# Kernel optimization log

Measured on AMD Instinct MI355X. Metric: run time of the kernel, lower is better.

Reference implementation:

```python
import jax, jax.numpy as jnp
import numpy as np

DIM = 768
HEADS = 12
HID = 3072  # mlp_ratio * dim
BATCH = 8
FRAMES = 16
GRID = 14
NTOK = GRID * GRID
LN_EPS = 1e-5
EPS = 1e-6


def setup_inputs() -> dict:
    key = jax.random.key(0)
    ks = jax.random.split(key, 8)
    w = lambda k, shape: jax.random.normal(k, shape, jnp.float32) * 0.02
    return {
        "x": jax.random.normal(ks[0], (BATCH * FRAMES, NTOK, DIM), jnp.float32),
        "ln1_w": jnp.ones((DIM,), jnp.float32),
        "ln1_b": jnp.zeros((DIM,), jnp.float32),
        "qkv_w": w(ks[1], (3 * DIM, DIM)),
        "proj_w": w(ks[2], (DIM, DIM)),
        "proj_b": jnp.zeros((DIM,), jnp.float32),
        "ln2_w": jnp.ones((DIM,), jnp.float32),
        "ln2_b": jnp.zeros((DIM,), jnp.float32),
        "fc1_w": w(ks[3], (HID, DIM)),
        "fc1_b": jnp.zeros((HID,), jnp.float32),
        "dw_w": w(ks[4], (HID, 1, 3, 3)),
        "dw_b": jnp.zeros((HID,), jnp.float32),
        "fc2_w": w(ks[5], (DIM, HID)),
        "fc2_b": jnp.zeros((DIM,), jnp.float32),
        "H": GRID,
        "W": GRID,
        "num_frames": FRAMES,
    }


def _layernorm(x, w, b):
    mu = jnp.mean(x, axis=-1, keepdims=True)
    var = jnp.mean(jnp.square(x - mu), axis=-1, keepdims=True)
    return (x - mu) * jax.lax.rsqrt(var + LN_EPS) * w + b


def _joint_ts_attention(xn, qkv_w, proj_w, proj_b, num_frames):
    # xn: (b*f, n, c)
    Bt, n, C = xn.shape
    h = HEADS
    e = C // h
    scale = e ** (-0.5)
    qkv = jnp.einsum('bnc,dc->bnd', xn, qkv_w).reshape(Bt, n, 3, h, e)
    q, k, v = qkv[:, :, 0], qkv[:, :, 1], qkv[:, :, 2]
    # ReLU feature map + scale offset
    q_ = jax.nn.relu(q) + scale
    k_ = jax.nn.relu(k) + scale
    b = Bt // num_frames
    m = num_frames * n  # joint time-space sequence length
    q_ = q_.reshape(b, m, h, e)
    k_ = k_.reshape(b, m, h, e)
    v_ = v.reshape(b, m, h, e)
    # kv_: (b, h, e, e)
    kv = jnp.einsum('bnhe,bnhd->bhed', k_, v_)
    k_sum = jnp.sum(k_, axis=1)  # (b, h, e)
    z = 1.0 / (jnp.einsum('bnhe,bhe->bnh', q_, k_sum) + EPS)  # (b, m, h)
    out = jnp.einsum('bnhe,bhed->bnhd', q_, kv) * z[..., None]  # (b, m, h, e)
    out = out.reshape(Bt, n, C)
    return jnp.einsum('bnc,dc->bnd', out, proj_w) + proj_b


def _dwconv(x, w, b, H, W):
    # x: (B, N, C) -> NCHW depthwise 3x3, pad 1
    Bn, n, c = x.shape
    xi = jnp.transpose(x, (0, 2, 1)).reshape(Bn, c, H, W)
    y = jax.lax.conv_general_dilated(
        xi, w, window_strides=(1, 1), padding=((1, 1), (1, 1)),
        dimension_numbers=('NCHW', 'OIHW', 'NCHW'), feature_group_count=c)
    y = y + b[None, :, None, None]
    return jnp.transpose(y.reshape(Bn, c, n), (0, 2, 1))


def reference(x, ln1_w, ln1_b, qkv_w, proj_w, proj_b, ln2_w, ln2_b,
              fc1_w, fc1_b, dw_w, dw_b, fc2_w, fc2_b, H, W, num_frames):
    # x = x + attn(norm1(x), num_frames)
    x = x + _joint_ts_attention(_layernorm(x, ln1_w, ln1_b), qkv_w, proj_w, proj_b, num_frames)
    # x = x + mlp(norm2(x), H, W)
    xn = _layernorm(x, ln2_w, ln2_b)
    hdn = jnp.einsum('bnc,hc->bnh', xn, fc1_w) + fc1_b
    hdn = _dwconv(hdn, dw_w, dw_b, H, W)
    hdn = jax.nn.gelu(hdn, approximate=False)
    out = jnp.einsum('bnh,ch->bnc', hdn, fc2_w) + fc2_b
    return x + out
```

## Files before the change

kernel.cpp:

```cpp
#include <hip/hip_runtime.h>

typedef unsigned short u16;
typedef unsigned int u32;

typedef __bf16 bf16x8 __attribute__((ext_vector_type(8)));
typedef float f32x4 __attribute__((ext_vector_type(4)));

#define DIM 768
#define HID 3072
#define NTOK 196
#define BT 128
#define NTOKENS (BT * NTOK)
#define MJ 3136
#define HEADS 12

#define SZ_WB   ((size_t)(2304*768 + 768*768 + 3072*768 + 768*3072) * 2)
#define SZ_XN   ((size_t)NTOKENS * DIM * 2)
#define SZ_QKV  ((size_t)NTOKENS * 2304 * 2)
#define SZ_X2   ((size_t)NTOKENS * DIM * 4)
#define SZ_HDN  ((size_t)NTOKENS * HID * 2)
#define SZ_KV   ((size_t)96 * 4096 * 4)
#define SZ_KS   ((size_t)96 * 64 * 4)
#define WS_NEED (SZ_WB + SZ_XN + SZ_QKV + SZ_X2 + SZ_HDN + SZ_KV + SZ_KS)

static void* g_buf = nullptr;

__device__ __forceinline__ float b2f(u16 u) {
  union { u32 i; float f; } x; x.i = ((u32)u) << 16; return x.f;
}
__device__ __forceinline__ u16 f2b(float f) {
  u32 x = __float_as_uint(f);
  return (u16)((x + 0x7fffu + ((x >> 16) & 1u)) >> 16);
}

__device__ __forceinline__ void gload_lds16(const u16* g, u16* l) {
  __builtin_amdgcn_global_load_lds(
      (const __attribute__((address_space(1))) u32*)g,
      (__attribute__((address_space(3))) u32*)l, 16, 0, 0);
}

__global__ __launch_bounds__(256) void cvt_f32_bf16(const float* __restrict__ in,
    u16* __restrict__ out, int n4)
{
  int i = blockIdx.x * 256 + threadIdx.x;
  if (i < n4) {
    float4 f = ((const float4*)in)[i];
    ushort4 r;
    r.x = f2b(f.x); r.y = f2b(f.y); r.z = f2b(f.z); r.w = f2b(f.w);
    ((ushort4*)out)[i] = r;
  }
}

__global__ __launch_bounds__(256) void zero_f32(float* __restrict__ p, int n) {
  int i = blockIdx.x * 256 + threadIdx.x;
  if (i < n) p[i] = 0.0f;
}

__global__ __launch_bounds__(256) void ln_kernel(const float* __restrict__ xin,
    const float* __restrict__ w, const float* __restrict__ b, u16* __restrict__ out)
{
  const int token = blockIdx.x * 4 + (threadIdx.x >> 6);
  const int lane = threadIdx.x & 63;
  float v[12];
  const float* x = xin + (size_t)token * DIM;
#pragma unroll
  for (int c = 0; c < 3; ++c) {
    float4 f = *(const float4*)(x + c * 256 + lane * 4);
    v[c*4+0] = f.x; v[c*4+1] = f.y; v[c*4+2] = f.z; v[c*4+3] = f.w;
  }
  float s = 0.f, sq = 0.f;
#pragma unroll
  for (int i = 0; i < 12; ++i) { s += v[i]; sq += v[i] * v[i]; }
#pragma unroll
  for (int off = 32; off > 0; off >>= 1) {
    s += __shfl_xor(s, off, 64);
    sq += __shfl_xor(sq, off, 64);
  }
  const float mean = s * (1.0f / 768.0f);
  const float var = sq * (1.0f / 768.0f) - mean * mean;
  const float rstd = rsqrtf(var + 1e-5f);
  u16* o = out + (size_t)token * DIM;
#pragma unroll
  for (int c = 0; c < 3; ++c) {
    float4 wv = *(const float4*)(w + c * 256 + lane * 4);
    float4 bv = *(const float4*)(b + c * 256 + lane * 4);
    ushort4 r;
    r.x = f2b((v[c*4+0] - mean) * rstd * wv.x + bv.x);
    r.y = f2b((v[c*4+1] - mean) * rstd * wv.y + bv.y);
    r.z = f2b((v[c*4+2] - mean) * rstd * wv.z + bv.z);
    r.w = f2b((v[c*4+3] - mean) * rstd * wv.w + bv.w);
    *(ushort4*)(o + c * 256 + lane * 4) = r;
  }
}

template<int MODE, int NXT, int NN, int KK>
__global__ __launch_bounds__(512, 2) void gemm8(
    const u16* __restrict__ A, const u16* __restrict__ W,
    const float* __restrict__ bias, const float* __restrict__ res,
    void* __restrict__ out)
{
  extern __shared__ char smem[];
  u16* As = (u16*)smem;
  u16* Bs = (u16*)(smem + 65536);

  const int t = threadIdx.x;
  const int l = t & 63;
  const int w = t >> 6;
  const int wm = w >> 2;
  const int wn = w & 3;

  constexpr int TOTAL = 98 * NXT;
  constexpr int Q8 = TOTAL >> 3;
  constexpr int R8 = TOTAL & 7;
  const int orig = blockIdx.x;
  const int xcd = orig & 7;
  const int idx = orig >> 3;
  const int wg = (xcd < R8) ? (xcd * (Q8 + 1) + idx)
                            : (R8 * (Q8 + 1) + (xcd - R8) * Q8 + idx);
  const int m0 = (wg / NXT) * 256;
  const int n0 = (wg % NXT) * 256;

  const int srow = w * 16 + (l >> 3);
  const int scol = ((l & 7) ^ (l >> 3)) * 8;
  const u16* gA = A + (size_t)(m0 + srow) * KK + scol;
  const u16* gB = W + (size_t)(n0 + srow) * KK + scol;
  u16* lA = As + w * 1024;
  u16* lB = Bs + w * 1024;

#define STAGE_A(bb, h, kt) do { \
    const u16* g_ = gA + (size_t)(h) * 128 * KK + (size_t)(kt) * 64; \
    u16* l_ = lA + (bb) * 16384 + (h) * 8192; \
    gload_lds16(g_, l_); \
    gload_lds16(g_ + (size_t)8 * KK, l_ + 512); } while (0)
#define STAGE_B(bb, h, kt) do { \
    const u16* g_ = gB + (size_t)(h) * 128 * KK + (size_t)(kt) * 64; \
    u16* l_ = lB + (bb) * 16384 + (h) * 8192; \
    gload_lds16(g_, l_); \
    gload_lds16(g_ + (size_t)8 * KK, l_ + 512); } while (0)

  const int lm = l & 15;
  const int qq = l >> 4;
  const int acol = (qq << 4) ^ ((l & 7) << 4);
  const int abase = (wm * 128 + lm) * 128 + acol;
  const int bbase = (wn * 64 + lm) * 128 + acol;

  f32x4 acc[8][4];
#pragma unroll
  for (int mi = 0; mi < 8; ++mi)
#pragma unroll
    for (int ni = 0; ni < 4; ++ni) acc[mi][ni] = (f32x4){0.f, 0.f, 0.f, 0.f};

  constexpr int NT = KK / 64;

  STAGE_A(0, 0, 0); STAGE_A(0, 1, 0); STAGE_B(0, 0, 0); STAGE_B(0, 1, 0);
  STAGE_A(1, 0, 1); STAGE_A(1, 1, 1);
  asm volatile("s_waitcnt vmcnt(4)" ::: "memory");
  __builtin_amdgcn_s_barrier();

  for (int ti = 0; ti < NT; ++ti) {
    const int cb = ti & 1, nb = cb ^ 1;
    const char* Ac = (const char*)As + cb * 32768;
    const char* Bc = (const char*)Bs + cb * 32768;
    bf16x8 a0[4][2], a1[4][2], b01[2][2], b23[2][2];

#pragma unroll
    for (int mi = 0; mi < 4; ++mi) {
      const int off = abase + mi * 2048;
      a0[mi][0] = *(const bf16x8*)(Ac + off);
      a0[mi][1] = *(const bf16x8*)(Ac + (off ^ 64));
    }
#pragma unroll
    for (int ni = 0; ni < 2; ++ni) {
      const int off = bbase + ni * 2048;
      b01[ni][0] = *(const bf16x8*)(Bc + off);
      b01[ni][1] = *(const bf16x8*)(Bc + (off ^ 64));
    }
    if (ti + 1 < NT) STAGE_B(nb, 0, ti + 1);
    __builtin_amdgcn_s_setprio(1);
#pragma unroll
    for (int mi = 0; mi < 4; ++mi)
#pragma unroll
      for (int ni = 0; ni < 2; ++ni) {
        acc[mi][ni] = __builtin_amdgcn_mfma_f32_16x16x32_bf16(a0[mi][0], b01[ni][0], acc[mi][ni], 0, 0, 0);
        acc[mi][ni] = __builtin_amdgcn_mfma_f32_16x16x32_bf16(a0[mi][1], b01[ni][1], acc[mi][ni], 0, 0, 0);
      }
    __builtin_amdgcn_s_setprio(0);

#pragma unroll
    for (int ni = 0; ni < 2; ++ni) {
      const int off = bbase + (ni + 2) * 2048;
      b23[ni][0] = *(const bf16x8*)(Bc + off);
      b23[ni][1] = *(const bf16x8*)(Bc + (off ^ 64));
    }
    if (ti + 1 < NT) STAGE_B(nb, 1, ti + 1);
    __builtin_amdgcn_s_setprio(1);
#pragma unroll
    for (int mi = 0; mi < 4; ++mi)
#pragma unroll
      for (int ni = 0; ni < 2; ++ni) {
        acc[mi][ni + 2] = __builtin_amdgcn_mfma_f32_16x16x32_bf16(a0[mi][0], b23[ni][0], acc[mi][ni + 2], 0, 0, 0);
        acc[mi][ni + 2] = __builtin_amdgcn_mfma_f32_16x16x32_bf16(a0[mi][1], b23[ni][1], acc[mi][ni + 2], 0, 0, 0);
      }
    __builtin_amdgcn_s_setprio(0);

#pragma unroll
    for (int mi = 0; mi < 4; ++mi) {
      const int off = abase + 8192 + mi * 2048;
      a1[mi][0] = *(const bf16x8*)(Ac + off);
      a1[mi][1] = *(const bf16x8*)(Ac + (off ^ 64));
    }
    __builtin_amdgcn_s_setprio(1);
#pragma unroll
    for (int mi = 0; mi < 4; ++mi)
#pragma unroll
      for (int ni = 0; ni < 2; ++ni) {
        acc[mi + 4][ni + 2] = __builtin_amdgcn_mfma_f32_16x16x32_bf16(a1[mi][0], b23[ni][0], acc[mi + 4][ni + 2], 0, 0, 0);
        acc[mi + 4][ni + 2] = __builtin_amdgcn_mfma_f32_16x16x32_bf16(a1[mi][1], b23[ni][1], acc[mi + 4][ni + 2], 0, 0, 0);
      }
    __builtin_amdgcn_s_setprio(0);

    asm volatile("s_waitcnt lgkmcnt(0)" ::: "memory");
    __builtin_amdgcn_s_barrier();

    if (ti + 2 < NT) { STAGE_A(cb, 0, ti + 2); STAGE_A(cb, 1, ti + 2); }

    __builtin_amdgcn_s_setprio(1);
#pragma unroll
    for (int mi = 0; mi < 4; ++mi)
#pragma unroll
      for (int ni = 0; ni < 2; ++ni) {
        acc[mi + 4][ni] = __builtin_amdgcn_mfma_f32_16x16x32_bf16(a1[mi][0], b01[ni][0], acc[mi + 4][ni], 0, 0, 0);
        acc[mi + 4][ni] = __builtin_amdgcn_mfma_f32_16x16x32_bf16(a1[mi][1], b01[ni][1], acc[mi + 4][ni], 0, 0, 0);
      }
    __builtin_amdgcn_s_setprio(0);

    if (ti + 2 < NT) {
      asm volatile("s_waitcnt vmcnt(4)" ::: "memory");
    } else {
      asm volatile("s_waitcnt vmcnt(0)" ::: "memory");
    }
    __builtin_amdgcn_s_barrier();
  }
#undef STAGE_A
#undef STAGE_B

#pragma unroll
  for (int mi = 0; mi < 8; ++mi) {
    const int rbase = m0 + wm * 128 + mi * 16 + qq * 4;
#pragma unroll
    for (int ni = 0; ni < 4; ++ni) {
      const int col = n0 + wn * 64 + ni * 16 + lm;
      float bv = 0.f;
      if (MODE != 0) bv = bias[col];
#pragma unroll
      for (int r = 0; r < 4; ++r) {
        float v = acc[mi][ni][r];
        const size_t idxo = (size_t)(rbase + r) * NN + col;
        if (MODE == 0) {
          if (col < 1536) v = fmaxf(v, 0.0f) + 0.125f;
          ((u16*)out)[idxo] = f2b(v);
        } else if (MODE == 1) {
          ((float*)out)[idxo] = v + bv + res[idxo];
        } else if (MODE == 2) {
          ((u16*)out)[idxo] = f2b(v + bv);
        } else {
          ((float*)out)[idxo] = v + bv + res[idxo];
        }
      }
    }
  }
}

__global__ __launch_bounds__(256) void kv_reduce(const u16* __restrict__ qkv,
    float* __restrict__ kv, float* __restrict__ ksum)
{
  const int bh = blockIdx.x;
  const int s = blockIdx.y;
  const int b = bh / 12, h = bh % 12;
  __shared__ __align__(16) u16 ks[64 * 64];
  __shared__ __align__(16) u16 vs[64 * 64];
  const int t = threadIdx.x;
  const int e = t & 63;
  const int dg = (t >> 6) * 16;

  float acc[16];
#pragma unroll
  for (int j = 0; j < 16; ++j) acc[j] = 0.f;
  float ksacc = 0.f;

  for (int ch = s; ch < 49; ch += 8) {
    const size_t tokbase = (size_t)b * MJ + ch * 64;
    __syncthreads();
#pragma unroll
    for (int i = 0; i < 2; ++i) {
      int c = t + i * 256;
      int row = c >> 3, eo = (c & 7) * 8;
      const u16* base = qkv + (tokbase + row) * 2304 + h * 64 + eo;
      *(uint4*)&ks[row * 64 + eo] = *(const uint4*)(base + 768);
      *(uint4*)&vs[row * 64 + eo] = *(const uint4*)(base + 1536);
    }
    __syncthreads();
    for (int m = 0; m < 64; ++m) {
      float kf = b2f(ks[m * 64 + e]);
      ksacc += kf;
      bf16x8 v0 = *(const bf16x8*)&vs[m * 64 + dg];
      bf16x8 v1 = *(const bf16x8*)&vs[m * 64 + dg + 8];
#pragma unroll
      for (int j = 0; j < 8; ++j) {
        acc[j]     += kf * (float)v0[j];
        acc[j + 8] += kf * (float)v1[j];
      }
    }
  }
  float* dst = kv + (size_t)bh * 4096 + e * 64 + dg;
#pragma unroll
  for (int j = 0; j < 16; ++j) atomicAdd(&dst[j], acc[j]);
  if (dg == 0) atomicAdd(&ksum[bh * 64 + e], ksacc);
}

__global__ __launch_bounds__(256) void attn_out(const u16* __restrict__ qkv,
    const float* __restrict__ kv, const float* __restrict__ ksum,
    u16* __restrict__ outp)
{
  const int chunk = blockIdx.x;
  const int h = blockIdx.y;
  const int b = blockIdx.z;
  __shared__ float kvs[4096];
  __shared__ float kss[64];
  __shared__ float qs[4096];
  const int t = threadIdx.x;
  const float* kvsrc = kv + (size_t)(b * 12 + h) * 4096;
  for (int i = t; i < 1024; i += 256)
    ((float4*)kvs)[i] = ((const float4*)kvsrc)[i];
  if (t < 64) kss[t] = ksum[(b * 12 + h) * 64 + t];
  __syncthreads();
  const int wv = t >> 6, lane = t & 63;
  float* qw = &qs[wv * 1024];
  const size_t tok0 = (size_t)b * MJ + chunk * 64 + wv * 16;
#pragma unroll
  for (int i = 0; i < 16; ++i) {
    float q = b2f(qkv[(tok0 + i) * 2304 + h * 64 + lane]);
    float pd = q * kss[lane];
#pragma unroll
    for (int off = 32; off > 0; off >>= 1) pd += __shfl_xor(pd, off, 64);
    qw[i * 64 + lane] = q * (1.0f / (pd + 1e-6f));
  }
  float o[16];
#pragma unroll
  for (int i = 0; i < 16; ++i) o[i] = 0.f;
  for (int e = 0; e < 64; ++e) {
    const float kvc = kvs[e * 64 + lane];
#pragma unroll
    for (int i = 0; i < 16; ++i) o[i] += qw[i * 64 + e] * kvc;
  }
#pragma unroll
  for (int i = 0; i < 16; ++i)
    outp[(tok0 + i) * 768 + h * 64 + lane] = f2b(o[i]);
}

__global__ __launch_bounds__(256) void dwconv_gelu(u16* __restrict__ hdn,
    const float* __restrict__ w, const float* __restrict__ bias)
{
  __shared__ u16 pl[196 * 136];
  const int cb = blockIdx.x;
  const int fr = blockIdx.y;
  const int t = threadIdx.x;
  const int c0 = cb * 128;
  u16* base = hdn + (size_t)fr * 196 * HID + c0;
#pragma unroll
  for (int i = 0; i < 13; ++i) {
    int idx = i * 256 + t;
    if (idx < 3136) {
      int p = idx >> 4, cq = idx & 15;
      *(uint4*)&pl[p * 136 + cq * 8] = *(const uint4*)(base + (size_t)p * HID + cq * 8);
    }
  }
  __syncthreads();
  const int pc = t & 31;
  const int pg = t >> 5;
  const int cc = pc * 4;
  float wr[36];
#pragma unroll
  for (int k = 0; k < 9; ++k)
#pragma unroll
    for (int u = 0; u < 4; ++u) wr[k * 4 + u] = w[(c0 + cc + u) * 9 + k];
  float bv[4];
#pragma unroll
  for (int u = 0; u < 4; ++u) bv[u] = bias[c0 + cc + u];

  for (int j = 0; j < 25; ++j) {
    const int p = pg + j * 8;
    if (p >= 196) break;
    const int py = p / 14, px = p % 14;
    float a0 = bv[0], a1 = bv[1], a2 = bv[2], a3 = bv[3];
#pragma unroll
    for (int ky = 0; ky < 3; ++ky) {
      int yy = py + ky - 1;
      if (yy < 0 || yy > 13) continue;
#pragma unroll
      for (int kx = 0; kx < 3; ++kx) {
        int xx = px + kx - 1;
        if (xx < 0 || xx > 13) continue;
        ushort4 tv = *(const ushort4*)&pl[(yy * 14 + xx) * 136 + cc];
        const float* wk = &wr[(ky * 3 + kx) * 4];
        a0 += wk[0] * b2f(tv.x);
        a1 += wk[1] * b2f(tv.y);
        a2 += wk[2] * b2f(tv.z);
        a3 += wk[3] * b2f(tv.w);
      }
    }
    ushort4 r;
    r.x = f2b(0.5f * a0 * (1.0f + erff(a0 * 0.70710678118654752f)));
    r.y = f2b(0.5f * a1 * (1.0f + erff(a1 * 0.70710678118654752f)));
    r.z = f2b(0.5f * a2 * (1.0f + erff(a2 * 0.70710678118654752f)));
    r.w = f2b(0.5f * a3 * (1.0f + erff(a3 * 0.70710678118654752f)));
    *(ushort4*)(base + (size_t)p * HID + cc) = r;
  }
}

static void set_gemm_attrs() {
  (void)hipFuncSetAttribute(reinterpret_cast<const void*>(&gemm8<0, 9, 2304, 768>),
                            hipFuncAttributeMaxDynamicSharedMemorySize, 131072);
  (void)hipFuncSetAttribute(reinterpret_cast<const void*>(&gemm8<1, 3, 768, 768>),
                            hipFuncAttributeMaxDynamicSharedMemorySize, 131072);
  (void)hipFuncSetAttribute(reinterpret_cast<const void*>(&gemm8<2, 12, 3072, 768>),
                            hipFuncAttributeMaxDynamicSharedMemorySize, 131072);
  (void)hipFuncSetAttribute(reinterpret_cast<const void*>(&gemm8<3, 3, 768, 3072>),
                            hipFuncAttributeMaxDynamicSharedMemorySize, 131072);
}
struct WsInit {
  WsInit() {
    (void)hipMalloc(&g_buf, WS_NEED);
    set_gemm_attrs();
  }
};
static WsInit g_wsinit;

extern "C" void kernel_launch(void* const* d_in, const int* in_sizes, int n_in,
                              void* d_out, int out_size, void* d_ws, size_t ws_size,
                              hipStream_t stream)
{
  (void)in_sizes; (void)n_in; (void)out_size;
  static bool attrs_once = [] { set_gemm_attrs(); return true; }();
  (void)attrs_once;

  const float* x     = (const float*)d_in[0];
  const float* ln1w  = (const float*)d_in[1];
  const float* ln1b  = (const float*)d_in[2];
  const float* qkvw  = (const float*)d_in[3];
  const float* projw = (const float*)d_in[4];
  const float* projb = (const float*)d_in[5];
  const float* ln2w  = (const float*)d_in[6];
  const float* ln2b  = (const float*)d_in[7];
  const float* fc1w  = (const float*)d_in[8];
  const float* fc1b  = (const float*)d_in[9];
  const float* dww   = (const float*)d_in[10];
  const float* dwb   = (const float*)d_in[11];
  const float* fc2w  = (const float*)d_in[12];
  const float* fc2b  = (const float*)d_in[13];

  char* p = (ws_size >= WS_NEED) ? (char*)d_ws : (char*)g_buf;
  u16* WQKV  = (u16*)p;   p += (size_t)2304 * 768 * 2;
  u16* WPROJ = (u16*)p;   p += (size_t)768 * 768 * 2;
  u16* WFC1  = (u16*)p;   p += (size_t)3072 * 768 * 2;
  u16* WFC2  = (u16*)p;   p += (size_t)768 * 3072 * 2;
  u16* XN    = (u16*)p;   p += SZ_XN;
  u16* QKV   = (u16*)p;   p += SZ_QKV;
  float* X2  = (float*)p; p += SZ_X2;
  u16* HDN   = (u16*)p;   p += SZ_HDN;
  float* KV  = (float*)p; p += SZ_KV;
  float* KS  = (float*)p; p += SZ_KS;

  cvt_f32_bf16<<<(2304*768/4 + 255)/256, 256, 0, stream>>>(qkvw, WQKV, 2304*768/4);
  cvt_f32_bf16<<<(768*768/4 + 255)/256, 256, 0, stream>>>(projw, WPROJ, 768*768/4);
  cvt_f32_bf16<<<(3072*768/4 + 255)/256, 256, 0, stream>>>(fc1w, WFC1, 3072*768/4);
  cvt_f32_bf16<<<(768*3072/4 + 255)/256, 256, 0, stream>>>(fc2w, WFC2, 768*3072/4);

  const int nz = 96 * 4096 + 96 * 64;
  zero_f32<<<(nz + 255) / 256, 256, 0, stream>>>(KV, nz);
  ln_kernel<<<NTOKENS / 4, 256, 0, stream>>>(x, ln1w, ln1b, XN);
  gemm8<0, 9, 2304, 768><<<98 * 9, 512, 131072, stream>>>(XN, WQKV, nullptr, nullptr, QKV);
  kv_reduce<<<dim3(96, 8), 256, 0, stream>>>(QKV, KV, KS);
  attn_out<<<dim3(49, 12, 8), 256, 0, stream>>>(QKV, KV, KS, XN);
  gemm8<1, 3, 768, 768><<<98 * 3, 512, 131072, stream>>>(XN, WPROJ, projb, x, X2);
  ln_kernel<<<NTOKENS / 4, 256, 0, stream>>>(X2, ln2w, ln2b, QKV);
  gemm8<2, 12, 3072, 768><<<98 * 12, 512, 131072, stream>>>(QKV, WFC1, fc1b, nullptr, HDN);
  dwconv_gelu<<<dim3(24, 128), 256, 0, stream>>>(HDN, dww, dwb);
  gemm8<3, 3, 768, 3072><<<98 * 3, 512, 131072, stream>>>(HDN, WFC2, fc2b, X2, (float*)d_out);
}
```

Baseline: 1.067 ms.

## Store K/V transposed from QKV GEMM and compute KV via MFMA

```diff
diff --git a/kernel.cpp b/kernel.cpp
--- a/kernel.cpp
+++ b/kernel.cpp
@@ -13,6 +13,8 @@
 #define NTOKENS (BT * NTOK)
 #define MJ 3136
 #define HEADS 12
+
+#define QB_ELE ((size_t)NTOKENS * 768)
 
 #define SZ_WB   ((size_t)(2304*768 + 768*768 + 3072*768 + 768*3072) * 2)
 #define SZ_XN   ((size_t)NTOKENS * DIM * 2)
@@ -247,78 +249,112 @@
 #pragma unroll
   for (int mi = 0; mi < 8; ++mi) {
     const int rbase = m0 + wm * 128 + mi * 16 + qq * 4;
+    const int b = rbase / 3136;
+    const int mj = rbase - b * 3136;
 #pragma unroll
     for (int ni = 0; ni < 4; ++ni) {
       const int col = n0 + wn * 64 + ni * 16 + lm;
-      float bv = 0.f;
-      if (MODE != 0) bv = bias[col];
-#pragma unroll
-      for (int r = 0; r < 4; ++r) {
-        float v = acc[mi][ni][r];
-        const size_t idxo = (size_t)(rbase + r) * NN + col;
-        if (MODE == 0) {
-          if (col < 1536) v = fmaxf(v, 0.0f) + 0.125f;
-          ((u16*)out)[idxo] = f2b(v);
-        } else if (MODE == 1) {
-          ((float*)out)[idxo] = v + bv + res[idxo];
-        } else if (MODE == 2) {
-          ((u16*)out)[idxo] = f2b(v + bv);
+      if (MODE == 0) {
+        if (col < 768) {
+#pragma unroll
+          for (int r = 0; r < 4; ++r) {
+            float v = fmaxf(acc[mi][ni][r], 0.0f) + 0.125f;
+            ((u16*)out)[(size_t)(rbase + r) * 768 + col] = f2b(v);
+          }
         } else {
-          ((float*)out)[idxo] = v + bv + res[idxo];
+          const bool isV = (col >= 1536);
+          const int cc = col - (isV ? 1536 : 768);
+          const int h = cc >> 6, e = cc & 63;
+          ushort4 pk;
+          float v0 = acc[mi][ni][0], v1 = acc[mi][ni][1];
+          float v2 = acc[mi][ni][2], v3 = acc[mi][ni][3];
+          if (!isV) {
+            v0 = fmaxf(v0, 0.0f) + 0.125f; v1 = fmaxf(v1, 0.0f) + 0.125f;
+            v2 = fmaxf(v2, 0.0f) + 0.125f; v3 = fmaxf(v3, 0.0f) + 0.125f;
+          }
+          pk.x = f2b(v0); pk.y = f2b(v1); pk.z = f2b(v2); pk.w = f2b(v3);
+          u16* dst = (u16*)out + (isV ? 2 * QB_ELE : QB_ELE)
+                   + ((size_t)((b * 12 + h) * 64 + e)) * 3136 + mj;
+          *(ushort4*)dst = pk;
         }
-      }
-    }
-  }
-}
-
-__global__ __launch_bounds__(256) void kv_reduce(const u16* __restrict__ qkv,
-    float* __restrict__ kv, float* __restrict__ ksum)
+      } else {
+        const float bv = bias[col];
+#pragma unroll
+        for (int r = 0; r < 4; ++r) {
+          float v = acc[mi][ni][r];
+          const size_t idxo = (size_t)(rbase + r) * NN + col;
+          if (MODE == 1) {
+            ((float*)out)[idxo] = v + bv + res[idxo];
+          } else if (MODE == 2) {
+            ((u16*)out)[idxo] = f2b(v + bv);
+          } else {
+            ((float*)out)[idxo] = v + bv + res[idxo];
+          }
+        }
+      }
+    }
+  }
+}
+
+__global__ __launch_bounds__(256) void ksum_kernel(const u16* __restrict__ KT,
+    float* __restrict__ KS)
+{
+  const int bh = blockIdx.x;
+  const int t = threadIdx.x;
+  const int w = t >> 6, l = t & 63;
+  const u16* base = KT + (size_t)(bh * 64 + w * 16) * 3136;
+  for (int r = 0; r < 16; ++r) {
+    float s = 0.f;
+    const u16* row = base + (size_t)r * 3136;
+#pragma unroll
+    for (int p = 0; p < 7; ++p) {
+      const int m = p * 512 + l * 8;
+      if (m < 3136) {
+        bf16x8 v = *(const bf16x8*)(row + m);
+#pragma unroll
+        for (int j = 0; j < 8; ++j) s += (float)v[j];
+      }
+    }
+#pragma unroll
+    for (int off = 32; off > 0; off >>= 1) s += __shfl_xor(s, off, 64);
+    if (l == 0) KS[bh * 64 + w * 16 + r] = s;
+  }
+}
+
+__global__ __launch_bounds__(256) void kv_mfma(const u16* __restrict__ KT,
+    const u16* __restrict__ VT, float* __restrict__ kv)
 {
   const int bh = blockIdx.x;
   const int s = blockIdx.y;
-  const int b = bh / 12, h = bh % 12;
-  __shared__ __align__(16) u16 ks[64 * 64];
-  __shared__ __align__(16) u16 vs[64 * 64];
   const int t = threadIdx.x;
-  const int e = t & 63;
-  const int dg = (t >> 6) * 16;
-
-  float acc[16];
-#pragma unroll
-  for (int j = 0; j < 16; ++j) acc[j] = 0.f;
-  float ksacc = 0.f;
-
-  for (int ch = s; ch < 49; ch += 8) {
-    const size_t tokbase = (size_t)b * MJ + ch * 64;
-    __syncthreads();
-#pragma unroll
-    for (int i = 0; i < 2; ++i) {
-      int c = t + i * 256;
-      int row = c >> 3, eo = (c & 7) * 8;
-      const u16* base = qkv + (tokbase + row) * 2304 + h * 64 + eo;
-      *(uint4*)&ks[row * 64 + eo] = *(const uint4*)(base + 768);
-      *(uint4*)&vs[row * 64 + eo] = *(const uint4*)(base + 1536);
-    }
-    __syncthreads();
-    for (int m = 0; m < 64; ++m) {
-      float kf = b2f(ks[m * 64 + e]);
-      ksacc += kf;
-      bf16x8 v0 = *(const bf16x8*)&vs[m * 64 + dg];
-      bf16x8 v1 = *(const bf16x8*)&vs[m * 64 + dg + 8];
-#pragma unroll
-      for (int j = 0; j < 8; ++j) {
-        acc[j]     += kf * (float)v0[j];
-        acc[j + 8] += kf * (float)v1[j];
-      }
-    }
-  }
-  float* dst = kv + (size_t)bh * 4096 + e * 64 + dg;
-#pragma unroll
-  for (int j = 0; j < 16; ++j) atomicAdd(&dst[j], acc[j]);
-  if (dg == 0) atomicAdd(&ksum[bh * 64 + e], ksacc);
-}
-
-__global__ __launch_bounds__(256) void attn_out(const u16* __restrict__ qkv,
+  const int l = t & 63, w = t >> 6;
+  const int lm = l & 15, qq = l >> 4;
+  const size_t mj0 = (size_t)s * 448;
+  const u16* ka = KT + (size_t)(bh * 64 + w * 16 + lm) * 3136 + mj0 + qq * 8;
+  const u16* vb = VT + (size_t)(bh * 64 + lm) * 3136 + mj0 + qq * 8;
+
+  f32x4 acc[4];
+#pragma unroll
+  for (int ni = 0; ni < 4; ++ni) acc[ni] = (f32x4){0.f, 0.f, 0.f, 0.f};
+
+#pragma unroll 4
+  for (int kk = 0; kk < 14; ++kk) {
+    bf16x8 a = *(const bf16x8*)(ka + kk * 32);
+#pragma unroll
+    for (int ni = 0; ni < 4; ++ni) {
+      bf16x8 b = *(const bf16x8*)(vb + (size_t)ni * 16 * 3136 + kk * 32);
+      acc[ni] = __builtin_amdgcn_mfma_f32_16x16x32_bf16(a, b, acc[ni], 0, 0, 0);
+    }
+  }
+  float* dst = kv + (size_t)bh * 4096;
+#pragma unroll
+  for (int ni = 0; ni < 4; ++ni)
+#pragma unroll
+    for (int r = 0; r < 4; ++r)
+      atomicAdd(&dst[(w * 16 + qq * 4 + r) * 64 + ni * 16 + lm], acc[ni][r]);
+}
+
+__global__ __launch_bounds__(256) void attn_out(const u16* __restrict__ qb,
     const float* __restrict__ kv, const float* __restrict__ ksum,
     u16* __restrict__ outp)
 {
@@ -339,7 +375,7 @@
   const size_t tok0 = (size_t)b * MJ + chunk * 64 + wv * 16;
 #pragma unroll
   for (int i = 0; i < 16; ++i) {
-    float q = b2f(qkv[(tok0 + i) * 2304 + h * 64 + lane]);
+    float q = b2f(qb[(tok0 + i) * 768 + h * 64 + lane]);
     float pd = q * kss[lane];
 #pragma unroll
     for (int off = 32; off > 0; off >>= 1) pd += __shfl_xor(pd, off, 64);
@@ -471,16 +507,20 @@
   float* KV  = (float*)p; p += SZ_KV;
   float* KS  = (float*)p; p += SZ_KS;
 
+  u16* KT = QKV + QB_ELE;
+  u16* VT = QKV + 2 * QB_ELE;
+
   cvt_f32_bf16<<<(2304*768/4 + 255)/256, 256, 0, stream>>>(qkvw, WQKV, 2304*768/4);
   cvt_f32_bf16<<<(768*768/4 + 255)/256, 256, 0, stream>>>(projw, WPROJ, 768*768/4);
   cvt_f32_bf16<<<(3072*768/4 + 255)/256, 256, 0, stream>>>(fc1w, WFC1, 3072*768/4);
   cvt_f32_bf16<<<(768*3072/4 + 255)/256, 256, 0, stream>>>(fc2w, WFC2, 768*3072/4);
 
-  const int nz = 96 * 4096 + 96 * 64;
+  const int nz = 96 * 4096;
   zero_f32<<<(nz + 255) / 256, 256, 0, stream>>>(KV, nz);
   ln_kernel<<<NTOKENS / 4, 256, 0, stream>>>(x, ln1w, ln1b, XN);
   gemm8<0, 9, 2304, 768><<<98 * 9, 512, 131072, stream>>>(XN, WQKV, nullptr, nullptr, QKV);
-  kv_reduce<<<dim3(96, 8), 256, 0, stream>>>(QKV, KV, KS);
+  ksum_kernel<<<96, 256, 0, stream>>>(KT, KS);
+  kv_mfma<<<dim3(96, 7), 256, 0, stream>>>(KT, VT, KV);
   attn_out<<<dim3(49, 12, 8), 256, 0, stream>>>(QKV, KV, KS, XN);
   gemm8<1, 3, 768, 768><<<98 * 3, 512, 131072, stream>>>(XN, WPROJ, projb, x, X2);
   ln_kernel<<<NTOKENS / 4, 256, 0, stream>>>(X2, ln2w, ln2b, QKV);
```

Measured after the change: 895.9 us. 16.0% less time.
